# Kernel tuning notes

Measured on AMD Instinct MI355X. Metric: run time of the kernel, lower is better.

The kernel has to match this reference:

```python
import jax, jax.numpy as jnp
import numpy as np

N_NODES, N_EDGES, N_TRIP = 100000, 200000, 600000
HID, HEADS, RADIUS = 256, 8, 3
ATOM_F, BOND_F = 133, 14

def setup_inputs() -> dict:
    key = jax.random.key(0)
    ks = jax.random.split(key, 20)
    def w(k, i, o):
        return jax.random.normal(k, (i, o), dtype=jnp.float32) / np.sqrt(i)
    L = RADIUS - 1
    return {
        'atom_feature': jax.random.normal(ks[0], (N_NODES, ATOM_F), dtype=jnp.float32),
        'edge_feature': jax.random.normal(ks[1], (N_EDGES, BOND_F), dtype=jnp.float32),
        'W_i': w(ks[2], ATOM_F + BOND_F, HID),
        'Wq': jnp.stack([w(jax.random.fold_in(ks[3], l), HID, HID) for l in range(L)]),
        'Wk': jnp.stack([w(jax.random.fold_in(ks[4], l), HID, HID) for l in range(L)]),
        'Wv': jnp.stack([w(jax.random.fold_in(ks[5], l), HID, HID) for l in range(L)]),
        'L1w': jnp.stack([w(jax.random.fold_in(ks[6], l), HID, HID) for l in range(L)]),
        'L1b': jnp.zeros((L, HID), dtype=jnp.float32),
        'L2w': jnp.stack([w(jax.random.fold_in(ks[7], l), HID, HID) for l in range(L)]),
        'L2b': jnp.zeros((L, HID), dtype=jnp.float32),
        'Wo': w(ks[8], ATOM_F + HID, HID),
        'bo': jnp.zeros((HID,), dtype=jnp.float32),
        'src': jax.random.randint(ks[9], (N_EDGES,), 0, N_NODES, dtype=jnp.int32),
        'dst': jax.random.randint(ks[10], (N_EDGES,), 0, N_NODES, dtype=jnp.int32),
        'idx_kj': jax.random.randint(ks[11], (N_TRIP,), 0, N_EDGES, dtype=jnp.int32),
        'idx_ji': jax.random.randint(ks[12], (N_TRIP,), 0, N_EDGES, dtype=jnp.int32),
    }

def _att_layer(feats, Wq, Wk, Wv, l1w, l1b, l2w, l2b, idx_kj, idx_ji):
    E = feats.shape[0]
    d = HID // HEADS
    q = (feats @ Wq).reshape(E, HEADS, d)
    k = (feats @ Wk).reshape(E, HEADS, d)
    v = (feats @ Wv).reshape(E, HEADS, d)
    # per-triplet attention logits [T, heads, 1]
    att = jnp.sum(q[idx_kj] * k[idx_ji], axis=-1, keepdims=True)
    att = jnp.exp(jax.nn.leaky_relu(att, negative_slope=0.2))
    denom = jax.ops.segment_sum(att, idx_ji, num_segments=E)  # edge softmax norm
    att = att / denom[idx_ji]
    v_att = (v[idx_kj] * att).reshape(-1, HID)
    v_flat = v.reshape(E, HID)
    # v_clone = v + index_add(v_att) - v == segment_sum of messages
    v_clone = jax.ops.segment_sum(v_att, idx_ji, num_segments=E)
    # residual MLP (dropout p=0 -> identity)
    h = jax.nn.relu(jax.nn.relu(v_clone @ l1w + l1b) @ l2w + l2b)
    return v_flat + h

def reference(atom_feature, edge_feature, W_i, Wq, Wk, Wv, L1w, L1b, L2w, L2b, Wo, bo, src, dst, idx_kj, idx_ji):
    # per-edge initial feature: concat(src atom feature, edge feature)
    init = jnp.concatenate([atom_feature[src], edge_feature], axis=1)
    feats = jax.nn.relu(init @ W_i)
    for l in range(RADIUS - 1):
        feats = _att_layer(feats, Wq[l], Wk[l], Wv[l], L1w[l], L1b[l], L2w[l], L2b[l], idx_kj, idx_ji)
    # edge -> node sum (dgl update_all copy_e + sum onto dst)
    feats_sum = jax.ops.segment_sum(feats, dst, num_segments=atom_feature.shape[0])
    a_input = jnp.concatenate([atom_feature, feats_sum], axis=1)
    return jax.nn.relu(a_input @ Wo + bo)
```

## Files before the change

### kernel.cpp

```cpp
#include <hip/hip_runtime.h>
#include <stdint.h>

#define NN 100000
#define NNP 100096
#define NE 200000
#define NEP 200064
#define NT 600000
#define HID 256

typedef __attribute__((ext_vector_type(8))) short bf16x8;
typedef __attribute__((ext_vector_type(4))) float f32x4;

__device__ __forceinline__ float bf2f(unsigned short u) {
    union { unsigned int i; float f; } x; x.i = ((unsigned int)u) << 16; return x.f;
}
__device__ __forceinline__ unsigned short f2bf(float f) {
    union { float f; unsigned int i; } x; x.f = f;
    unsigned int r = (x.i + 0x7FFFu + ((x.i >> 16) & 1u)) >> 16;
    return (unsigned short)r;
}

__device__ __forceinline__ void gload16(const void* g, void* l) {
    __builtin_amdgcn_global_load_lds(
        (const __attribute__((address_space(1))) void*)g,
        (__attribute__((address_space(3))) void*)l, 16, 0, 0);
}

template<int FLAGS, bool CBF>
__device__ __forceinline__
void gemm128_core(const unsigned short* __restrict__ A,
                  const unsigned short* __restrict__ BT,
                  const float* __restrict__ bias,
                  const unsigned short* __restrict__ res,
                  void* __restrict__ Cv, int row0, int col0,
                  int Mreal, int Kpad,
                  unsigned short* Asb, unsigned short* Bsb)
{
    const int t    = threadIdx.x;
    const int lane = t & 63;
    const int wv   = t >> 6;
    const int wr   = wv >> 1;
    const int wc   = wv & 1;
    const int l15  = lane & 15;
    const int lk   = lane >> 4;
    const int sub  = lane >> 3;
    const int schk = lane & 7;

    f32x4 acc[4][4];
#pragma unroll
    for (int i = 0; i < 4; ++i)
#pragma unroll
        for (int j = 0; j < 4; ++j) acc[i][j] = (f32x4){0.f, 0.f, 0.f, 0.f};

    const int nt = Kpad >> 6;
    for (int kt = 0; kt < nt; ++kt) {
        const int k0 = kt << 6;
#pragma unroll
        for (int j = 0; j < 4; ++j) {
            const int ii = wv * 4 + j;
            const int r  = ii * 8 + sub;
            const int cg = schk ^ (r & 7);
            gload16(A + (size_t)(row0 + r) * Kpad + k0 + cg * 8, Asb + ii * 512);
        }
#pragma unroll
        for (int j = 0; j < 4; ++j) {
            const int ii = wv * 4 + j;
            const int r  = ii * 8 + sub;
            const int cg = schk ^ (r & 7);
            gload16(BT + (size_t)(col0 + r) * Kpad + k0 + cg * 8, Bsb + ii * 512);
        }
        __syncthreads();
#pragma unroll
        for (int ks = 0; ks < 2; ++ks) {
            bf16x8 af[4], bfg[4];
#pragma unroll
            for (int mi = 0; mi < 4; ++mi) {
                const int r = wr * 64 + mi * 16 + l15;
                const int c = ks * 4 + lk;
                af[mi] = *(const bf16x8*)((const char*)Asb
                          + r * 128 + ((c ^ (r & 7)) << 4));
            }
#pragma unroll
            for (int ni = 0; ni < 4; ++ni) {
                const int r = wc * 64 + ni * 16 + l15;
                const int c = ks * 4 + lk;
                bfg[ni] = *(const bf16x8*)((const char*)Bsb
                           + r * 128 + ((c ^ (r & 7)) << 4));
            }
#pragma unroll
            for (int mi = 0; mi < 4; ++mi)
#pragma unroll
                for (int ni = 0; ni < 4; ++ni)
                    acc[mi][ni] = __builtin_amdgcn_mfma_f32_16x16x32_bf16(
                        af[mi], bfg[ni], acc[mi][ni], 0, 0, 0);
        }
        __syncthreads();
    }

#pragma unroll
    for (int mi = 0; mi < 4; ++mi) {
#pragma unroll
        for (int r = 0; r < 4; ++r) {
            const int row = row0 + wr * 64 + mi * 16 + lk * 4 + r;
            if (row >= Mreal) continue;
#pragma unroll
            for (int ni = 0; ni < 4; ++ni) {
                const int col = col0 + wc * 64 + ni * 16 + l15;
                float o = acc[mi][ni][r];
                if (FLAGS & 2) o += bias[col];
                if (FLAGS & 1) o = fmaxf(o, 0.f);
                if (FLAGS & 4) o += bf2f(res[(size_t)row * HID + col]);
                if (CBF) ((unsigned short*)Cv)[(size_t)row * HID + col] = f2bf(o);
                else     ((float*)Cv)[(size_t)row * HID + col] = o;
            }
        }
    }
}

template<int FLAGS, bool CBF>
__global__ __launch_bounds__(256, 4)
void gemm128(const unsigned short* __restrict__ A,
             const unsigned short* __restrict__ BT,
             const float* __restrict__ bias,
             const unsigned short* __restrict__ res,
             void* __restrict__ Cv, int Mtiles, int Mreal, int Kpad)
{
    __shared__ alignas(16) unsigned short Asb[128 * 64];
    __shared__ alignas(16) unsigned short Bsb[128 * 64];
    const int x   = blockIdx.x;
    const int xcd = x & 7;
    const int ii  = x >> 3;
    const int g   = (ii >> 1) * 8 + xcd;
    const int ch  = ii & 1;
    if (g >= Mtiles) return;
    gemm128_core<FLAGS, CBF>(A, BT, bias, res, Cv, g * 128, ch * 128,
                             Mreal, Kpad, Asb, Bsb);
}

__global__ __launch_bounds__(256, 4)
void gemm128_qkv(const unsigned short* __restrict__ A,
                 const unsigned short* __restrict__ BTq,
                 const unsigned short* __restrict__ BTk,
                 const unsigned short* __restrict__ BTv,
                 unsigned short* __restrict__ Cq,
                 unsigned short* __restrict__ Ck,
                 unsigned short* __restrict__ Cvp, int Mtiles)
{
    __shared__ alignas(16) unsigned short Asb[128 * 64];
    __shared__ alignas(16) unsigned short Bsb[128 * 64];
    const int x   = blockIdx.x;
    const int xcd = x & 7;
    const int ii  = x >> 3;
    const int g   = (ii / 6) * 8 + xcd;
    const int j   = ii % 6;
    if (g >= Mtiles) return;
    const int proj = j >> 1;
    const int ch   = j & 1;
    const unsigned short* BT = (proj == 0) ? BTq : (proj == 1) ? BTk : BTv;
    unsigned short*       C  = (proj == 0) ? Cq  : (proj == 1) ? Ck  : Cvp;
    gemm128_core<0, true>(A, BT, nullptr, nullptr, C, g * 128, ch * 128,
                          NE, 256, Asb, Bsb);
}

__global__ __launch_bounds__(256)
void wconv(const float* __restrict__ W, unsigned short* __restrict__ BT,
           int Kreal, int Kpad)
{
    const int idx = blockIdx.x * 256 + threadIdx.x;
    const int n = idx / Kpad, kp = idx - n * Kpad;
    float v = (kp < Kreal) ? W[(size_t)kp * HID + n] : 0.f;
    BT[idx] = f2bf(v);
}

__global__ __launch_bounds__(256)
void wconv10(const float* __restrict__ Wq, const float* __restrict__ Wk,
             const float* __restrict__ Wv, const float* __restrict__ L1w,
             const float* __restrict__ L2w, unsigned short* __restrict__ outbase)
{
    const int y = blockIdx.y;
    const int l = y / 5, which = y - l * 5;
    const float* src;
    switch (which) {
        case 0: src = Wq;  break;
        case 1: src = Wk;  break;
        case 2: src = Wv;  break;
        case 3: src = L1w; break;
        default: src = L2w; break;
    }
    src += (size_t)l * 65536;
    const int idx = blockIdx.x * 256 + threadIdx.x;
    const int n = idx >> 8, kp = idx & 255;
    outbase[(size_t)y * 65536 + idx] = f2bf(src[(size_t)kp * HID + n]);
}

__global__ __launch_bounds__(256)
void build_initA(const float* __restrict__ atom, const float* __restrict__ edge,
                 const int* __restrict__ src, unsigned short* __restrict__ out)
{
    const long total = (long)NE * 192;
    long idx = (long)blockIdx.x * blockDim.x + threadIdx.x;
    if (idx >= total) return;
    const int e = (int)(idx / 192);
    const int c = (int)(idx - (long)e * 192);
    float v = 0.f;
    if (c < 133)      v = atom[(size_t)src[e] * 133 + c];
    else if (c < 147) v = edge[(size_t)e * 14 + (c - 133)];
    out[idx] = f2bf(v);
}

__global__ __launch_bounds__(256)
void build_finalA(const float* __restrict__ atom, const float* __restrict__ fsum,
                  unsigned short* __restrict__ out)
{
    const long total = (long)NNP * 448;
    long idx = (long)blockIdx.x * blockDim.x + threadIdx.x;
    if (idx >= total) return;
    const int n = (int)(idx / 448);
    const int c = (int)(idx - (long)n * 448);
    float v = 0.f;
    if (n < NN) {
        if (c < 133)      v = atom[(size_t)n * 133 + c];
        else if (c < 389) v = fsum[(size_t)n * 256 + (c - 133)];
    }
    out[idx] = f2bf(v);
}

__global__ __launch_bounds__(256)
void count_keys(const int* __restrict__ key, int n, int nkeys, int* __restrict__ cnt)
{
    const int i = blockIdx.x * 256 + threadIdx.x;
    if (i < n) {
        const int kk = key[i];
        if ((unsigned)kk < (unsigned)nkeys) atomicAdd(&cnt[kk], 1);
    }
}

__global__ __launch_bounds__(256)
void fill_trip(const int* __restrict__ idx_ji, const int* __restrict__ idx_kj,
               int* __restrict__ cur, int* __restrict__ plist)
{
    const int i = blockIdx.x * 256 + threadIdx.x;
    if (i >= NT) return;
    const int kk = idx_ji[i];
    if ((unsigned)kk >= (unsigned)NE) return;
    const int pos = atomicAdd(&cur[kk], 1);
    if ((unsigned)pos < (unsigned)NT) plist[pos] = idx_kj[i];
}

__global__ __launch_bounds__(256)
void fill_node(const int* __restrict__ dst, int* __restrict__ cur,
               int* __restrict__ plist)
{
    const int i = blockIdx.x * 256 + threadIdx.x;
    if (i >= NE) return;
    const int kk = dst[i];
    if ((unsigned)kk >= (unsigned)NN) return;
    const int pos = atomicAdd(&cur[NE + kk], 1);
    if ((unsigned)pos < (unsigned)(NT + NE)) plist[pos] = i;
}

__global__ __launch_bounds__(256)
void scan1(const int* __restrict__ in, int n, int* __restrict__ excl,
           int* __restrict__ part)
{
    __shared__ int sh[256];
    const int t = threadIdx.x;
    const int base = blockIdx.x * 2048 + t * 8;
    int v[8]; int s = 0;
#pragma unroll
    for (int j = 0; j < 8; ++j) { v[j] = (base + j < n) ? in[base + j] : 0; s += v[j]; }
    sh[t] = s; __syncthreads();
    for (int off = 1; off < 256; off <<= 1) {
        int x = (t >= off) ? sh[t - off] : 0;
        __syncthreads();
        sh[t] += x;
        __syncthreads();
    }
    int ex = sh[t] - s;
#pragma unroll
    for (int j = 0; j < 8; ++j) { if (base + j < n) excl[base + j] = ex; ex += v[j]; }
    if (t == 255) part[blockIdx.x] = sh[255];
}

__global__ __launch_bounds__(256)
void scan2(int* __restrict__ part, int nparts)
{
    __shared__ int sh[256];
    const int t = threadIdx.x;
    const int v = (t < nparts) ? part[t] : 0;
    sh[t] = v; __syncthreads();
    for (int off = 1; off < 256; off <<= 1) {
        int x = (t >= off) ? sh[t - off] : 0;
        __syncthreads();
        sh[t] += x;
        __syncthreads();
    }
    if (t < nparts) part[t] = sh[t] - v;
}

__global__ __launch_bounds__(256)
void scan3(const int* __restrict__ excl, const int* __restrict__ part,
           const int* counts, int n, int* __restrict__ offs, int* cur)
{
    const int i = blockIdx.x * 256 + threadIdx.x;
    if (i >= n) return;
    const int v = excl[i] + part[i >> 11];
    const int c = counts[i];
    offs[i] = v;
    cur[i] = v;
    if (i == n - 1) offs[n] = v + c;
}

__global__ __launch_bounds__(256)
void gather_v(const unsigned short* __restrict__ q, const unsigned short* __restrict__ k,
              const unsigned short* __restrict__ v,
              const int* __restrict__ toff, const int* __restrict__ tkj,
              unsigned short* __restrict__ vc)
{
    const long gtid = (long)blockIdx.x * blockDim.x + threadIdx.x;
    const int w    = (int)(gtid >> 5);
    const int lane = threadIdx.x & 31;
    if (w >= NE) return;
    int beg = toff[w], end = toff[w + 1];
    if (beg < 0) beg = 0;
    if (end > NT) end = NT;

    const bf16x8 kv = *(const bf16x8*)(k + (size_t)w * HID + lane * 8);
    float kf[8];
#pragma unroll
    for (int j = 0; j < 8; ++j) kf[j] = bf2f((unsigned short)kv[j]);

    float av[8];
#pragma unroll
    for (int j = 0; j < 8; ++j) av[j] = 0.f;
    float den = 0.f;

    int kj_next = (beg < end) ? tkj[beg] : -1;
    for (int p = beg; p < end; ++p) {
        const int kj = kj_next;
        if (p + 1 < end) kj_next = tkj[p + 1];
        if ((unsigned)kj >= (unsigned)NE) continue;
        const bf16x8 qv = *(const bf16x8*)(q + (size_t)kj * HID + lane * 8);
        float s = 0.f;
#pragma unroll
        for (int j = 0; j < 8; ++j) s += bf2f((unsigned short)qv[j]) * kf[j];
        s += __shfl_xor(s, 1);
        s += __shfl_xor(s, 2);
        const float lr = (s > 0.f) ? s : 0.2f * s;
        const float a  = __expf(lr);
        den += a;
        const bf16x8 vv = *(const bf16x8*)(v + (size_t)kj * HID + lane * 8);
#pragma unroll
        for (int j = 0; j < 8; ++j) av[j] += a * bf2f((unsigned short)vv[j]);
    }
    const float inv = (den != 0.f) ? 1.f / den : 0.f;
    bf16x8 o;
#pragma unroll
    for (int j = 0; j < 8; ++j) o[j] = (short)f2bf(av[j] * inv);
    *(bf16x8*)(vc + (size_t)w * HID + lane * 8) = o;
}

__global__ __launch_bounds__(256)
void gather_node(const unsigned short* __restrict__ feats,
                 const int* __restrict__ noff, const int* __restrict__ nlist,
                 float* __restrict__ fsum)
{
    const long gtid = (long)blockIdx.x * blockDim.x + threadIdx.x;
    const int w    = (int)(gtid >> 5);
    const int lane = threadIdx.x & 31;
    if (w >= NN) return;
    int beg = noff[w], end = noff[w + 1];
    if (beg < 0) beg = 0;
    if (end > NT + NE) end = NT + NE;
    float av[8];
#pragma unroll
    for (int j = 0; j < 8; ++j) av[j] = 0.f;
    int e_next = (beg < end) ? nlist[beg] : -1;
    for (int p = beg; p < end; ++p) {
        const int e = e_next;
        if (p + 1 < end) e_next = nlist[p + 1];
        if ((unsigned)e >= (unsigned)NE) continue;
        const bf16x8 f = *(const bf16x8*)(feats + (size_t)e * HID + lane * 8);
#pragma unroll
        for (int j = 0; j < 8; ++j) av[j] += bf2f((unsigned short)f[j]);
    }
    float4 o0 = make_float4(av[0], av[1], av[2], av[3]);
    float4 o1 = make_float4(av[4], av[5], av[6], av[7]);
    float* out = fsum + (size_t)w * HID + lane * 8;
    *reinterpret_cast<float4*>(out)     = o0;
    *reinterpret_cast<float4*>(out + 4) = o1;
}

extern "C" void kernel_launch(void* const* d_in, const int* in_sizes, int n_in,
                              void* d_out, int out_size, void* d_ws, size_t ws_size,
                              hipStream_t stream)
{
    const float* atom = (const float*)d_in[0];
    const float* edge = (const float*)d_in[1];
    const float* W_i  = (const float*)d_in[2];
    const float* Wq   = (const float*)d_in[3];
    const float* Wk   = (const float*)d_in[4];
    const float* Wv   = (const float*)d_in[5];
    const float* L1w  = (const float*)d_in[6];
    const float* L1b  = (const float*)d_in[7];
    const float* L2w  = (const float*)d_in[8];
    const float* L2b  = (const float*)d_in[9];
    const float* Wo   = (const float*)d_in[10];
    const float* bo   = (const float*)d_in[11];
    const int* src    = (const int*)d_in[12];
    const int* dst    = (const int*)d_in[13];
    const int* idx_kj = (const int*)d_in[14];
    const int* idx_ji = (const int*)d_in[15];

    const size_t RB = (size_t)NE * HID * 2;
    char* ws = (char*)d_ws;
    unsigned short* feats = (unsigned short*)(ws);
    unsigned short* qb    = (unsigned short*)(ws + RB);
    unsigned short* kb    = (unsigned short*)(ws + 2 * RB);
    unsigned short* vb    = (unsigned short*)d_out;
    unsigned short* vc    = feats;
    unsigned short* initA = qb;
    unsigned short* h1    = kb;
    float*          fsum  = (float*)(ws + RB);
    unsigned short* finalA = kb;

    const int NK = NE + NN;
    char* p = ws + 3 * RB;
    int* offs     = (int*)p; p += ((size_t)NK + 16) * 4;
    int* cur      = (int*)p; p += ((size_t)NK + 16) * 4;
    int* plist    = (int*)p; p += (size_t)(NT + NE) * 4;
    int* tmp_excl = (int*)p; p += ((size_t)NK + 16) * 4;
    int* partials = (int*)p; p += 1024;
    unsigned short* wiT = (unsigned short*)p; p += (size_t)256 * 192 * 2;
    unsigned short* wT0 = (unsigned short*)p; p += (size_t)10 * 65536 * 2;
    unsigned short* woT = (unsigned short*)p; p += (size_t)256 * 448 * 2;
    const size_t NEEDED = (size_t)(p - ws);
    if (ws_size < NEEDED) return;
    auto wT = [&](int i) { return wT0 + (size_t)i * 65536; };

    const int MT_E  = NEP / 128;
    const int MT_E8 = ((MT_E + 7) / 8) * 8;
    const int MT_N  = NNP / 128;
    const int MT_N8 = ((MT_N + 7) / 8) * 8;
    const int NPARTS = (NK + 2047) / 2048;

    wconv<<<192, 256, 0, stream>>>(W_i, wiT, 147, 192);
    wconv10<<<dim3(256, 10), 256, 0, stream>>>(Wq, Wk, Wv, L1w, L2w, wT0);
    wconv<<<448, 256, 0, stream>>>(Wo, woT, 389, 448);

    hipMemsetAsync(cur, 0, (size_t)NK * 4, stream);
    count_keys<<<(NT + 255) / 256, 256, 0, stream>>>(idx_ji, NT, NE, cur);
    count_keys<<<(NE + 255) / 256, 256, 0, stream>>>(dst, NE, NN, cur + NE);
    scan1<<<NPARTS, 256, 0, stream>>>(cur, NK, tmp_excl, partials);
    scan2<<<1, 256, 0, stream>>>(partials, NPARTS);
    scan3<<<(NK + 255) / 256, 256, 0, stream>>>(tmp_excl, partials, cur, NK, offs, cur);
    fill_trip<<<(NT + 255) / 256, 256, 0, stream>>>(idx_ji, idx_kj, cur, plist);
    fill_node<<<(NE + 255) / 256, 256, 0, stream>>>(dst, cur, plist);

    {
        const long total = (long)NE * 192;
        build_initA<<<(int)((total + 255) / 256), 256, 0, stream>>>(atom, edge, src, initA);
    }
    gemm128<1, true><<<MT_E8 * 2, 256, 0, stream>>>(initA, wiT, nullptr, nullptr,
                                                    feats, MT_E, NE, 192);

    for (int l = 0; l < 2; ++l) {
        const float* l1b = L1b + (size_t)l * 256;
        const float* l2b = L2b + (size_t)l * 256;

        gemm128_qkv<<<MT_E8 * 6, 256, 0, stream>>>(
            feats, wT(l * 5 + 0), wT(l * 5 + 1), wT(l * 5 + 2), qb, kb, vb, MT_E);

        gather_v<<<(NE * 32) / 256, 256, 0, stream>>>(qb, kb, vb, offs, plist, vc);

        gemm128<3, true><<<MT_E8 * 2, 256, 0, stream>>>(vc, wT(l * 5 + 3), l1b,
                                                        nullptr, h1, MT_E, NE, 256);
        gemm128<7, true><<<MT_E8 * 2, 256, 0, stream>>>(h1, wT(l * 5 + 4), l2b,
                                                        vb, feats, MT_E, NE, 256);
    }

    gather_node<<<(NN * 32) / 256, 256, 0, stream>>>(feats, offs + NE, plist, fsum);
    {
        const long total = (long)NNP * 448;
        build_finalA<<<(int)((total + 255) / 256), 256, 0, stream>>>(atom, fsum, finalA);
    }
    gemm128<3, false><<<MT_N8 * 2, 256, 0, stream>>>(finalA, woT, bo, nullptr,
                                                     d_out, MT_N, NN, 448);
}
```

Before: 1.278 ms.

## Make GEMM blocks persistent over multiple M-tiles and prefetch the next tile's first K-slice

Each GEMM block now walks several 128-row tiles (strided by 8 to keep XCD locality) instead of one, with T=4 for QKV and T=2 elsewhere. The loop is restructured so the global-to-LDS load for the next K-slice, or the next tile's first slice, is issued after the MFMA work, with the epilogue stores of the current tile overlapping that load. This aims to cut block launch and prologue overhead and hide some load latency. In exchange the grid is smaller, which can lower occupancy and parallelism across CUs, and it adds an extra barrier per K step.

```diff
diff --git a/kernel.cpp b/kernel.cpp
--- a/kernel.cpp
+++ b/kernel.cpp
@@ -28,33 +28,27 @@
 
 template<int FLAGS, bool CBF>
 __device__ __forceinline__
-void gemm128_core(const unsigned short* __restrict__ A,
-                  const unsigned short* __restrict__ BT,
-                  const float* __restrict__ bias,
-                  const unsigned short* __restrict__ res,
-                  void* __restrict__ Cv, int row0, int col0,
-                  int Mreal, int Kpad,
-                  unsigned short* Asb, unsigned short* Bsb)
-{
-    const int t    = threadIdx.x;
-    const int lane = t & 63;
-    const int wv   = t >> 6;
+void gemm128_mt_core(const unsigned short* __restrict__ A,
+                     const unsigned short* __restrict__ BT,
+                     const float* __restrict__ bias,
+                     const unsigned short* __restrict__ res,
+                     void* __restrict__ Cv,
+                     int g0, int T, int Mtiles, int col0,
+                     int Mreal, int Kpad,
+                     unsigned short* Asb, unsigned short* Bsb)
+{
+    const int tid  = threadIdx.x;
+    const int lane = tid & 63;
+    const int wv   = tid >> 6;
     const int wr   = wv >> 1;
     const int wc   = wv & 1;
     const int l15  = lane & 15;
     const int lk   = lane >> 4;
     const int sub  = lane >> 3;
     const int schk = lane & 7;
-
-    f32x4 acc[4][4];
-#pragma unroll
-    for (int i = 0; i < 4; ++i)
-#pragma unroll
-        for (int j = 0; j < 4; ++j) acc[i][j] = (f32x4){0.f, 0.f, 0.f, 0.f};
-
-    const int nt = Kpad >> 6;
-    for (int kt = 0; kt < nt; ++kt) {
-        const int k0 = kt << 6;
+    const int nt   = Kpad >> 6;
+
+    auto stage = [&](int row0, int k0) {
 #pragma unroll
         for (int j = 0; j < 4; ++j) {
             const int ii = wv * 4 + j;
@@ -69,50 +63,78 @@
             const int cg = schk ^ (r & 7);
             gload16(BT + (size_t)(col0 + r) * Kpad + k0 + cg * 8, Bsb + ii * 512);
         }
-        __syncthreads();
-#pragma unroll
-        for (int ks = 0; ks < 2; ++ks) {
-            bf16x8 af[4], bfg[4];
-#pragma unroll
-            for (int mi = 0; mi < 4; ++mi) {
-                const int r = wr * 64 + mi * 16 + l15;
-                const int c = ks * 4 + lk;
-                af[mi] = *(const bf16x8*)((const char*)Asb
-                          + r * 128 + ((c ^ (r & 7)) << 4));
+    };
+
+    f32x4 acc[4][4];
+#pragma unroll
+    for (int i = 0; i < 4; ++i)
+#pragma unroll
+        for (int j = 0; j < 4; ++j) acc[i][j] = (f32x4){0.f, 0.f, 0.f, 0.f};
+
+    stage(g0 * 128, 0);
+    __syncthreads();
+
+    for (int t = 0; t < T; ++t) {
+        const int g = g0 + t * 8;
+        if (g >= Mtiles) break;
+        const int row0 = g * 128;
+        for (int kt = 0; kt < nt; ++kt) {
+#pragma unroll
+            for (int ks = 0; ks < 2; ++ks) {
+                bf16x8 af[4], bfg[4];
+#pragma unroll
+                for (int mi = 0; mi < 4; ++mi) {
+                    const int r = wr * 64 + mi * 16 + l15;
+                    const int c = ks * 4 + lk;
+                    af[mi] = *(const bf16x8*)((const char*)Asb
+                              + r * 128 + ((c ^ (r & 7)) << 4));
+                }
+#pragma unroll
+                for (int ni = 0; ni < 4; ++ni) {
+                    const int r = wc * 64 + ni * 16 + l15;
+                    const int c = ks * 4 + lk;
+                    bfg[ni] = *(const bf16x8*)((const char*)Bsb
+                               + r * 128 + ((c ^ (r & 7)) << 4));
+                }
+#pragma unroll
+                for (int mi = 0; mi < 4; ++mi)
+#pragma unroll
+                    for (int ni = 0; ni < 4; ++ni)
+                        acc[mi][ni] = __builtin_amdgcn_mfma_f32_16x16x32_bf16(
+                            af[mi], bfg[ni], acc[mi][ni], 0, 0, 0);
             }
-#pragma unroll
-            for (int ni = 0; ni < 4; ++ni) {
-                const int r = wc * 64 + ni * 16 + l15;
-                const int c = ks * 4 + lk;
-                bfg[ni] = *(const bf16x8*)((const char*)Bsb
-                           + r * 128 + ((c ^ (r & 7)) << 4));
+            __syncthreads();
+
+            if (kt != nt - 1) {
+                stage(row0, (kt + 1) << 6);
+            } else {
+                const int gn = g + 8;
+                if (t + 1 < T && gn < Mtiles) stage(gn * 128, 0);
+#pragma unroll
+                for (int mi = 0; mi < 4; ++mi) {
+#pragma unroll
+                    for (int r = 0; r < 4; ++r) {
+                        const int row = row0 + wr * 64 + mi * 16 + lk * 4 + r;
+                        if (row < Mreal) {
+#pragma unroll
+                            for (int ni = 0; ni < 4; ++ni) {
+                                const int col = col0 + wc * 64 + ni * 16 + l15;
+                                float o = acc[mi][ni][r];
+                                if (FLAGS & 2) o += bias[col];
+                                if (FLAGS & 1) o = fmaxf(o, 0.f);
+                                if (FLAGS & 4) o += bf2f(res[(size_t)row * HID + col]);
+                                if (CBF) ((unsigned short*)Cv)[(size_t)row * HID + col] = f2bf(o);
+                                else     ((float*)Cv)[(size_t)row * HID + col] = o;
+                            }
+                        }
+                    }
+                }
+#pragma unroll
+                for (int i = 0; i < 4; ++i)
+#pragma unroll
+                    for (int j = 0; j < 4; ++j) acc[i][j] = (f32x4){0.f, 0.f, 0.f, 0.f};
             }
-#pragma unroll
-            for (int mi = 0; mi < 4; ++mi)
-#pragma unroll
-                for (int ni = 0; ni < 4; ++ni)
-                    acc[mi][ni] = __builtin_amdgcn_mfma_f32_16x16x32_bf16(
-                        af[mi], bfg[ni], acc[mi][ni], 0, 0, 0);
-        }
-        __syncthreads();
-    }
-
-#pragma unroll
-    for (int mi = 0; mi < 4; ++mi) {
-#pragma unroll
-        for (int r = 0; r < 4; ++r) {
-            const int row = row0 + wr * 64 + mi * 16 + lk * 4 + r;
-            if (row >= Mreal) continue;
-#pragma unroll
-            for (int ni = 0; ni < 4; ++ni) {
-                const int col = col0 + wc * 64 + ni * 16 + l15;
-                float o = acc[mi][ni][r];
-                if (FLAGS & 2) o += bias[col];
-                if (FLAGS & 1) o = fmaxf(o, 0.f);
-                if (FLAGS & 4) o += bf2f(res[(size_t)row * HID + col]);
-                if (CBF) ((unsigned short*)Cv)[(size_t)row * HID + col] = f2bf(o);
-                else     ((float*)Cv)[(size_t)row * HID + col] = o;
-            }
+            __syncthreads();
         }
     }
 }
@@ -123,18 +145,19 @@
              const unsigned short* __restrict__ BT,
              const float* __restrict__ bias,
              const unsigned short* __restrict__ res,
-             void* __restrict__ Cv, int Mtiles, int Mreal, int Kpad)
+             void* __restrict__ Cv, int Mtiles, int Mreal, int Kpad, int T)
 {
     __shared__ alignas(16) unsigned short Asb[128 * 64];
     __shared__ alignas(16) unsigned short Bsb[128 * 64];
     const int x   = blockIdx.x;
     const int xcd = x & 7;
-    const int ii  = x >> 3;
-    const int g   = (ii >> 1) * 8 + xcd;
-    const int ch  = ii & 1;
-    if (g >= Mtiles) return;
-    gemm128_core<FLAGS, CBF>(A, BT, bias, res, Cv, g * 128, ch * 128,
-                             Mreal, Kpad, Asb, Bsb);
+    const int y   = x >> 3;
+    const int m   = y & 1;
+    const int c   = y >> 1;
+    const int g0  = c * T * 8 + xcd;
+    if (g0 >= Mtiles) return;
+    gemm128_mt_core<FLAGS, CBF>(A, BT, bias, res, Cv, g0, T, Mtiles, m * 128,
+                                Mreal, Kpad, Asb, Bsb);
 }
 
 __global__ __launch_bounds__(256, 4)
@@ -144,22 +167,23 @@
                  const unsigned short* __restrict__ BTv,
                  unsigned short* __restrict__ Cq,
                  unsigned short* __restrict__ Ck,
-                 unsigned short* __restrict__ Cvp, int Mtiles)
+                 unsigned short* __restrict__ Cvp, int Mtiles, int T)
 {
     __shared__ alignas(16) unsigned short Asb[128 * 64];
     __shared__ alignas(16) unsigned short Bsb[128 * 64];
     const int x   = blockIdx.x;
     const int xcd = x & 7;
-    const int ii  = x >> 3;
-    const int g   = (ii / 6) * 8 + xcd;
-    const int j   = ii % 6;
-    if (g >= Mtiles) return;
-    const int proj = j >> 1;
-    const int ch   = j & 1;
+    const int y   = x >> 3;
+    const int m   = y % 6;
+    const int c   = y / 6;
+    const int g0  = c * T * 8 + xcd;
+    if (g0 >= Mtiles) return;
+    const int proj = m >> 1;
+    const int ch   = m & 1;
     const unsigned short* BT = (proj == 0) ? BTq : (proj == 1) ? BTk : BTv;
     unsigned short*       C  = (proj == 0) ? Cq  : (proj == 1) ? Ck  : Cvp;
-    gemm128_core<0, true>(A, BT, nullptr, nullptr, C, g * 128, ch * 128,
-                          NE, 256, Asb, Bsb);
+    gemm128_mt_core<0, true>(A, BT, nullptr, nullptr, C, g0, T, Mtiles,
+                             ch * 128, NE, 256, Asb, Bsb);
 }
 
 __global__ __launch_bounds__(256)
@@ -439,10 +463,15 @@
     auto wT = [&](int i) { return wT0 + (size_t)i * 65536; };
 
     const int MT_E  = NEP / 128;
-    const int MT_E8 = ((MT_E + 7) / 8) * 8;
     const int MT_N  = NNP / 128;
-    const int MT_N8 = ((MT_N + 7) / 8) * 8;
     const int NPARTS = (NK + 2047) / 2048;
+
+    const int JE = (MT_E + 7) / 8;
+    const int JN = (MT_N + 7) / 8;
+    const int T_QKV = 4, T_G = 2;
+    const int GRID_QKV = 8 * 6 * ((JE + T_QKV - 1) / T_QKV);
+    const int GRID_E   = 8 * 2 * ((JE + T_G - 1) / T_G);
+    const int GRID_N   = 8 * 2 * ((JN + T_G - 1) / T_G);
 
     wconv<<<192, 256, 0, stream>>>(W_i, wiT, 147, 192);
     wconv10<<<dim3(256, 10), 256, 0, stream>>>(Wq, Wk, Wv, L1w, L2w, wT0);
@@ -461,22 +490,23 @@
         const long total = (long)NE * 192;
         build_initA<<<(int)((total + 255) / 256), 256, 0, stream>>>(atom, edge, src, initA);
     }
-    gemm128<1, true><<<MT_E8 * 2, 256, 0, stream>>>(initA, wiT, nullptr, nullptr,
-                                                    feats, MT_E, NE, 192);
+    gemm128<1, true><<<GRID_E, 256, 0, stream>>>(initA, wiT, nullptr, nullptr,
+                                                 feats, MT_E, NE, 192, T_G);
 
     for (int l = 0; l < 2; ++l) {
         const float* l1b = L1b + (size_t)l * 256;
         const float* l2b = L2b + (size_t)l * 256;
 
-        gemm128_qkv<<<MT_E8 * 6, 256, 0, stream>>>(
-            feats, wT(l * 5 + 0), wT(l * 5 + 1), wT(l * 5 + 2), qb, kb, vb, MT_E);
+        gemm128_qkv<<<GRID_QKV, 256, 0, stream>>>(
+            feats, wT(l * 5 + 0), wT(l * 5 + 1), wT(l * 5 + 2), qb, kb, vb,
+            MT_E, T_QKV);
 
         gather_v<<<(NE * 32) / 256, 256, 0, stream>>>(qb, kb, vb, offs, plist, vc);
 
-        gemm128<3, true><<<MT_E8 * 2, 256, 0, stream>>>(vc, wT(l * 5 + 3), l1b,
-                                                        nullptr, h1, MT_E, NE, 256);
-        gemm128<7, true><<<MT_E8 * 2, 256, 0, stream>>>(h1, wT(l * 5 + 4), l2b,
-                                                        vb, feats, MT_E, NE, 256);
+        gemm128<3, true><<<GRID_E, 256, 0, stream>>>(vc, wT(l * 5 + 3), l1b,
+                                                     nullptr, h1, MT_E, NE, 256, T_G);
+        gemm128<7, true><<<GRID_E, 256, 0, stream>>>(h1, wT(l * 5 + 4), l2b,
+                                                     vb, feats, MT_E, NE, 256, T_G);
     }
 
     gather_node<<<(NN * 32) / 256, 256, 0, stream>>>(feats, offs + NE, plist, fsum);
@@ -484,6 +514,6 @@
         const long total = (long)NNP * 448;
         build_finalA<<<(int)((total + 255) / 256), 256, 0, stream>>>(atom, fsum, finalA);
     }
-    gemm128<3, false><<<MT_N8 * 2, 256, 0, stream>>>(finalA, woT, bo, nullptr,
-                                                     d_out, MT_N, NN, 448);
-}
+    gemm128<3, false><<<GRID_N, 256, 0, stream>>>(finalA, woT, bo, nullptr,
+                                                  d_out, MT_N, NN, 448, T_G);
+}
```

Result: slower. 2.084 ms (+63.0%).
